# Kernel optimization log

Measured on AMD Instinct MI355X. Metric: run time of the kernel, lower is better.

Reference implementation:

```python
import jax, jax.numpy as jnp
import numpy as np

TARGET_SPARSITY = 0.9
LN_EPS = 1e-5


def ternary_quant(W):
    """BitNet-b1.58 style ternary quantization: W -> {-1,0,+1} * mean(|W|).
    Straight-through estimator so gradients pass to the latent weights."""
    scale = jnp.mean(jnp.abs(W))
    q = jnp.clip(jnp.round(W / (scale + 1e-8)), -1.0, 1.0) * scale
    return W + jax.lax.stop_gradient(q - W)


def layernorm(x, gamma, beta):
    mu = jnp.mean(x, axis=-1, keepdims=True)
    var = jnp.var(x, axis=-1, keepdims=True)
    return (x - mu) * jax.lax.rsqrt(var + LN_EPS) * gamma + beta


def setup_inputs() -> dict:
    key = jax.random.key(0)
    ks = jax.random.split(key, 3)
    B, S, D, N = 4, 2048, 2048, 8192
    x = jax.random.normal(ks[0], (B, S, D), dtype=jnp.float32)
    W_syn = jax.random.normal(ks[1], (N, D), dtype=jnp.float32) * (1.0 / np.sqrt(D))
    b_syn = jnp.zeros((N,), dtype=jnp.float32)
    W_out = jax.random.normal(ks[2], (D, N), dtype=jnp.float32) * (1.0 / np.sqrt(N))
    b_out = jnp.zeros((D,), dtype=jnp.float32)
    gamma = jnp.ones((D,), dtype=jnp.float32)
    beta = jnp.zeros((D,), dtype=jnp.float32)
    return {"x": x, "W_syn": W_syn, "b_syn": b_syn, "W_out": W_out,
            "b_out": b_out, "gamma": gamma, "beta": beta}


def reference(x, W_syn, b_syn, W_out, b_out, gamma, beta):
    B, S, D = x.shape
    N = W_syn.shape[0]
    x_flat = x.reshape(-1, D)  # [T, D], T = B*S

    # RNU: ternary-weight synapses + sparse firing (keep top (1-sparsity) per token)
    z = x_flat @ ternary_quant(W_syn).T + b_syn  # [T, N]
    k = max(1, int(N * (1.0 - TARGET_SPARSITY)))
    topv, _ = jax.lax.top_k(z, k)                 # [T, k]
    thresh = topv[:, -1:]                          # k-th largest per token
    hidden = jnp.where(z >= thresh, jax.nn.relu(z), 0.0)  # sparse firing rates

    # Ternary output projection
    out = hidden @ ternary_quant(W_out).T + b_out  # [T, D]
    out = out.reshape(B, S, D)

    # Residual + LayerNorm
    return layernorm(x + out, gamma, beta)
```

## Files before the change

### kernel.cpp

```cpp
#include <hip/hip_runtime.h>


typedef __attribute__((ext_vector_type(8))) short short8;
typedef __attribute__((ext_vector_type(4))) float f32x4;

__device__ __forceinline__ float bf2f(unsigned h) {
    return __uint_as_float(h << 16);
}
__device__ __forceinline__ unsigned f2bf(float f) {
    unsigned u = __float_as_uint(f);
    return (u + 0x7fffu + ((u >> 16) & 1u)) >> 16;
}

typedef __attribute__((address_space(1))) const void gq_void;
typedef __attribute__((address_space(3))) void ls_void;
__device__ __forceinline__ void gload16(const void* g, void* l) {
    __builtin_amdgcn_global_load_lds((gq_void*)g, (ls_void*)l, 16, 0, 0);
}

__global__ __launch_bounds__(64) void init_detect(float* sc, const unsigned* g_raw,
                                                  int* flag) {
    if (threadIdx.x < 16) sc[threadIdx.x] = 0.0f;
    if (threadIdx.x == 0) *flag = (g_raw[0] == 0x3F803F80u) ? 1 : 0;
}

__global__ __launch_bounds__(256) void split_x(const void* __restrict__ src,
                                               unsigned short* __restrict__ hi,
                                               unsigned short* __restrict__ lo, int n,
                                               const int* __restrict__ flagp) {
    const int flag = *flagp;
    int idx = blockIdx.x * 256 + threadIdx.x;
    int stride = gridDim.x * 256;
    if (flag) {
        const uint4* s = (const uint4*)src;
        uint4* dh = (uint4*)hi;
        uint4* dl = (uint4*)lo;
        uint4 zz; zz.x = zz.y = zz.z = zz.w = 0u;
        for (int i = idx; i < n / 8; i += stride) { dh[i] = s[i]; dl[i] = zz; }
    } else {
        const float4* s = (const float4*)src;
        uint2* dh = (uint2*)hi;
        uint2* dl = (uint2*)lo;
        for (int i = idx; i < n / 4; i += stride) {
            float4 v = s[i];
            unsigned h0 = f2bf(v.x), h1 = f2bf(v.y), h2 = f2bf(v.z), h3 = f2bf(v.w);
            unsigned l0 = f2bf(v.x - bf2f(h0));
            unsigned l1 = f2bf(v.y - bf2f(h1));
            unsigned l2 = f2bf(v.z - bf2f(h2));
            unsigned l3 = f2bf(v.w - bf2f(h3));
            uint2 oh; oh.x = h0 | (h1 << 16); oh.y = h2 | (h3 << 16);
            uint2 ol; ol.x = l0 | (l1 << 16); ol.y = l2 | (l3 << 16);
            dh[i] = oh;
            dl[i] = ol;
        }
    }
}

__global__ __launch_bounds__(256) void to_f32(const void* __restrict__ src,
                                              float* __restrict__ dst, int n,
                                              const int* __restrict__ flagp) {
    const int flag = *flagp;
    int i = blockIdx.x * 256 + threadIdx.x;
    if (i >= n) return;
    if (flag) dst[i] = bf2f((unsigned)((const unsigned short*)src)[i]);
    else dst[i] = ((const float*)src)[i];
}

__global__ __launch_bounds__(256) void abs_sum_any(const void* __restrict__ w, int n,
                                                   float* __restrict__ out,
                                                   const int* __restrict__ flagp) {
    const int flag = *flagp;
    int idx = blockIdx.x * 256 + threadIdx.x;
    int stride = gridDim.x * 256;
    float s = 0.0f;
    if (flag) {
        const uint4* wv = (const uint4*)w;
        for (int c = idx; c < n / 8; c += stride) {
            uint4 v = wv[c];
            unsigned a[4] = {v.x, v.y, v.z, v.w};
#pragma unroll
            for (int j = 0; j < 4; j++)
                s += fabsf(bf2f(a[j] & 0xffffu)) + fabsf(bf2f(a[j] >> 16));
        }
    } else {
        const float4* wv = (const float4*)w;
        for (int c = idx; c < n / 4; c += stride) {
            float4 v = wv[c];
            s += fabsf(v.x) + fabsf(v.y) + fabsf(v.z) + fabsf(v.w);
        }
    }
#pragma unroll
    for (int off = 32; off; off >>= 1) s += __shfl_down(s, off);
    __shared__ float red[4];
    int lane = threadIdx.x & 63, wv_id = threadIdx.x >> 6;
    if (lane == 0) red[wv_id] = s;
    __syncthreads();
    if (threadIdx.x == 0) atomicAdd(out, red[0] + red[1] + red[2] + red[3]);
}

__global__ __launch_bounds__(64) void finalize_scale(float* sc, float inv_count) {
    if (threadIdx.x == 0) {
        sc[2] = sc[0] * inv_count;
        sc[3] = sc[1] * inv_count;
    }
}

__global__ __launch_bounds__(256) void quantize_any(const void* __restrict__ w,
                                                    unsigned short* __restrict__ q,
                                                    const float* __restrict__ sc, int idx,
                                                    int n, const int* __restrict__ flagp) {
    const int flag = *flagp;
    const float d = sc[idx] + 1e-8f;
    int i = blockIdx.x * 256 + threadIdx.x;
    int stride = gridDim.x * 256;
    if (flag) {
        const uint4* wv = (const uint4*)w;
        uint4* qv = (uint4*)q;
        for (; i < n / 8; i += stride) {
            uint4 v = wv[i];
            unsigned a[4] = {v.x, v.y, v.z, v.w};
            unsigned r[4];
#pragma unroll
            for (int j = 0; j < 4; j++) {
                float lo = bf2f(a[j] & 0xffffu);
                float hi = bf2f(a[j] >> 16);
                float rl = fminf(1.0f, fmaxf(-1.0f, rintf(lo / d)));
                float rh = fminf(1.0f, fmaxf(-1.0f, rintf(hi / d)));
                r[j] = f2bf(rl) | (f2bf(rh) << 16);
            }
            uint4 o;
            o.x = r[0]; o.y = r[1]; o.z = r[2]; o.w = r[3];
            qv[i] = o;
        }
    } else {
        const float4* wv = (const float4*)w;
        uint2* qv = (uint2*)q;
        for (; i < n / 4; i += stride) {
            float4 v = wv[i];
            float r0 = fminf(1.0f, fmaxf(-1.0f, rintf(v.x / d)));
            float r1 = fminf(1.0f, fmaxf(-1.0f, rintf(v.y / d)));
            float r2 = fminf(1.0f, fmaxf(-1.0f, rintf(v.z / d)));
            float r3 = fminf(1.0f, fmaxf(-1.0f, rintf(v.w / d)));
            uint2 o;
            o.x = f2bf(r0) | (f2bf(r1) << 16);
            o.y = f2bf(r2) | (f2bf(r3) << 16);
            qv[i] = o;
        }
    }
}

template <int BM, int BN, bool TWO, int KSPLIT>
__global__ __launch_bounds__(256) void gemm_bt_t(const unsigned short* __restrict__ A0,
                                                 const unsigned short* __restrict__ A1,
                                                 const unsigned short* __restrict__ B,
                                                 float* __restrict__ C,
                                                 float* __restrict__ C2,
                                                 const float* __restrict__ biasf,
                                                 const float* __restrict__ scp, int scidx,
                                                 int N, int K) {
    constexpr int WM = BM / 2;
    constexpr int WN = BN / 2;
    constexpr int AM = WM / 16;
    constexpr int AN = WN / 16;
    __shared__ uint4 sA[BM * 8];
    __shared__ uint4 sL[TWO ? BM * 8 : 4];
    __shared__ uint4 sB[BN * 8];
    const int tid = threadIdx.x;
    const int lane = tid & 63;
    const int wave = tid >> 6;
    const int wm = (wave >> 1) * WM;
    const int wn = (wave & 1) * WN;
    const int m0 = blockIdx.y * BM;
    const int n0 = blockIdx.x * BN;
    const int l15 = lane & 15;
    const int quad = lane >> 4;

    const int kz = (KSPLIT > 1) ? (int)blockIdx.z : 0;
    const int kper = K / KSPLIT;
    const int kbeg = kz * kper;
    const int kend = kbeg + kper;
    float* __restrict__ Cw = (kz == 0) ? C : C2;

    f32x4 acc[AM][AN];
#pragma unroll
    for (int i = 0; i < AM; i++)
#pragma unroll
        for (int j = 0; j < AN; j++) acc[i][j] = (f32x4){0.f, 0.f, 0.f, 0.f};

    const unsigned short* Abase = A0 + (size_t)m0 * K;
    const unsigned short* Lbase = TWO ? (A1 + (size_t)m0 * K) : nullptr;
    const unsigned short* Bbase = B + (size_t)n0 * K;

    for (int k0 = kbeg; k0 < kend; k0 += 64) {
#pragma unroll
        for (int i = 0; i < BM * 8 / 256; i++) {
            int s = tid + i * 256;
            int r = s >> 3, c = s & 7;
            size_t go = (size_t)r * K + k0 + c * 8;
            gload16(Abase + go, sA + i * 256 + wave * 64);
            if (TWO) gload16(Lbase + go, sL + i * 256 + wave * 64);
        }
#pragma unroll
        for (int i = 0; i < BN * 8 / 256; i++) {
            int s = tid + i * 256;
            int r = s >> 3, c = s & 7;
            size_t go = (size_t)r * K + k0 + c * 8;
            gload16(Bbase + go, sB + i * 256 + wave * 64);
        }
        __syncthreads();
#pragma unroll
        for (int kk = 0; kk < 64; kk += 32) {
            const int jj = (kk >> 3) + quad;
            short8 ah[AM], bfr[AN];
#pragma unroll
            for (int t = 0; t < AM; t++)
                ah[t] = *(const short8*)&sA[(wm + t * 16 + l15) * 8 + jj];
#pragma unroll
            for (int t = 0; t < AN; t++)
                bfr[t] = *(const short8*)&sB[(wn + t * 16 + l15) * 8 + jj];
#pragma unroll
            for (int im = 0; im < AM; im++)
#pragma unroll
                for (int in = 0; in < AN; in++)
                    acc[im][in] = __builtin_amdgcn_mfma_f32_16x16x32_bf16(
                        ah[im], bfr[in], acc[im][in], 0, 0, 0);
            if (TWO) {
                short8 al[AM];
#pragma unroll
                for (int t = 0; t < AM; t++)
                    al[t] = *(const short8*)&sL[(wm + t * 16 + l15) * 8 + jj];
#pragma unroll
                for (int im = 0; im < AM; im++)
#pragma unroll
                    for (int in = 0; in < AN; in++)
                        acc[im][in] = __builtin_amdgcn_mfma_f32_16x16x32_bf16(
                            al[im], bfr[in], acc[im][in], 0, 0, 0);
            }
        }
        __syncthreads();
    }

    float scale = scp[scidx];
#pragma unroll
    for (int in = 0; in < AN; in++) {
        int col = n0 + wn + in * 16 + l15;
        float bv = (kz == 0) ? biasf[col] : 0.0f;
#pragma unroll
        for (int im = 0; im < AM; im++) {
            int rbase = m0 + wm + im * 16 + quad * 4;
#pragma unroll
            for (int r = 0; r < 4; r++) {
                Cw[(size_t)(rbase + r) * N + col] = scale * acc[im][in][r] + bv;
            }
        }
    }
}

__global__ __launch_bounds__(256) void topk_hidden(const float* __restrict__ z,
                                                   unsigned short* __restrict__ hidden,
                                                   int N, int k) {
    __shared__ unsigned keys[8192];
    __shared__ unsigned hist[2048];
    __shared__ unsigned csum[256];
    __shared__ unsigned sh_want, sh_kk;
    const int tid = threadIdx.x;
    const size_t row = blockIdx.x;
    const float* zr = z + row * (size_t)N;

    for (int i = tid; i < N; i += 256) {
        unsigned u = __float_as_uint(zr[i]);
        keys[i] = (u & 0x80000000u) ? ~u : (u | 0x80000000u);
    }
    if (tid == 0) { sh_want = 0u; sh_kk = (unsigned)k; }
    __syncthreads();

    for (int p = 0; p < 3; p++) {
        const int shift = (p == 0) ? 21 : (p == 1) ? 10 : 0;
        const int bits = (p == 2) ? 10 : 11;
        const int nb = 1 << bits;
        const unsigned want = sh_want;
        const unsigned kk = sh_kk;
        const int hs = shift + bits;
        for (int b = tid; b < nb; b += 256) hist[b] = 0u;
        __syncthreads();
        for (int i = tid; i < N; i += 256) {
            unsigned u = keys[i];
            bool match = (hs >= 32) ? true : ((u >> hs) == (want >> hs));
            if (match) atomicAdd(&hist[(u >> shift) & (nb - 1)], 1u);
        }
        __syncthreads();
        const int cs = nb >> 8;
        unsigned cv = 0;
        for (int j = 0; j < cs; j++) cv += hist[tid * cs + j];
        csum[tid] = cv;
        __syncthreads();
        for (int off = 1; off < 256; off <<= 1) {
            unsigned add = (tid + off < 256) ? csum[tid + off] : 0u;
            __syncthreads();
            csum[tid] += add;
            __syncthreads();
        }
        unsigned excl = (tid < 255) ? csum[tid + 1] : 0u;
        if (excl < kk && kk <= csum[tid]) {
            unsigned running = excl;
            for (int b = tid * cs + cs - 1; b >= tid * cs; b--) {
                unsigned h = hist[b];
                if (running + h >= kk) {
                    sh_want = want | ((unsigned)b << shift);
                    sh_kk = kk - running;
                    break;
                }
                running += h;
            }
        }
        __syncthreads();
    }

    const unsigned kth = sh_want;
    unsigned short* hr = hidden + row * (size_t)N;
    for (int i = tid; i < N; i += 256) {
        unsigned u = keys[i];
        float f = (u & 0x80000000u) ? __uint_as_float(u & 0x7fffffffu)
                                    : __uint_as_float(~u);
        float h = (u >= kth) ? fmaxf(f, 0.0f) : 0.0f;
        hr[i] = (unsigned short)f2bf(h);
    }
}

__global__ __launch_bounds__(256) void ln_kernel(const unsigned short* __restrict__ xh,
                                                 const unsigned short* __restrict__ xl,
                                                 const float* __restrict__ o,
                                                 const float* __restrict__ o2,
                                                 const float* __restrict__ gamma,
                                                 const float* __restrict__ beta,
                                                 float* __restrict__ y, int D) {
    const int tid = threadIdx.x;
    const size_t row = blockIdx.x;
    const unsigned short* xhr = xh + row * (size_t)D;
    const unsigned short* xlr = xl + row * (size_t)D;
    const float* orow = o + row * (size_t)D;
    const float* orow2 = o2 + row * (size_t)D;
    float v[8];
    float s = 0.0f, s2 = 0.0f;
#pragma unroll
    for (int j = 0; j < 8; j++) {
        int i = tid + j * 256;
        float val = bf2f((unsigned)xhr[i]) + bf2f((unsigned)xlr[i]) + orow[i] + orow2[i];
        v[j] = val;
        s += val;
        s2 += val * val;
    }
#pragma unroll
    for (int off = 32; off; off >>= 1) {
        s += __shfl_down(s, off);
        s2 += __shfl_down(s2, off);
    }
    __shared__ float red[8];
    int lane = tid & 63, wv = tid >> 6;
    if (lane == 0) { red[wv] = s; red[4 + wv] = s2; }
    __syncthreads();
    float S = red[0] + red[1] + red[2] + red[3];
    float S2 = red[4] + red[5] + red[6] + red[7];
    float mu = S / (float)D;
    float var = S2 / (float)D - mu * mu;
    float inv = rsqrtf(var + 1e-5f);
#pragma unroll
    for (int j = 0; j < 8; j++) {
        int i = tid + j * 256;
        y[row * (size_t)D + i] = (v[j] - mu) * inv * gamma[i] + beta[i];
    }
}

extern "C" void kernel_launch(void* const* d_in, const int* in_sizes, int n_in,
                              void* d_out, int out_size, void* d_ws, size_t ws_size,
                              hipStream_t stream) {
    const void* x_raw = d_in[0];
    const void* Wsyn_raw = d_in[1];
    const void* bsyn_raw = d_in[2];
    const void* Wout_raw = d_in[3];
    const void* bout_raw = d_in[4];
    const void* gamma_raw = d_in[5];
    const void* beta_raw = d_in[6];
    float* out = (float*)d_out;

    const int M = 8192, D = 2048, N = 8192, K1 = 2048;
    const int kTop = 819;
    const int NW = M * D;

    char* wsb = (char*)d_ws;
    float* sc = (float*)wsb;
    int* flag = (int*)(wsb + 128);
    float* gamma_f = (float*)(wsb + 4096);
    float* beta_f = (float*)(wsb + 12288);
    float* bout_f = (float*)(wsb + 20480);
    float* bsyn_f = (float*)(wsb + 28672);
    unsigned short* x_hi = (unsigned short*)(wsb + 65536);
    unsigned short* x_lo = (unsigned short*)(wsb + 65536 + 1ull * 33554432ull);
    unsigned short* qsyn = (unsigned short*)(wsb + 65536 + 2ull * 33554432ull);
    unsigned short* qout = (unsigned short*)(wsb + 65536 + 3ull * 33554432ull);
    const size_t FIXED = 65536 + 4ull * 33554432ull;

    const size_t per_row = (size_t)N * 4 + (size_t)N * 2;
    size_t avail = (ws_size > FIXED) ? ws_size - FIXED : 0;
    long mc = (long)(avail / per_row);
    mc &= ~127L;
    if (mc > M) mc = M;
    if (mc < 128) mc = 128;
    const int Mc = (int)mc;
    char* chunk_base = wsb + FIXED;

    init_detect<<<1, 64, 0, stream>>>(sc, (const unsigned*)gamma_raw, flag);

    split_x<<<2048, 256, 0, stream>>>(x_raw, x_hi, x_lo, M * D, flag);
    to_f32<<<(N + 255) / 256, 256, 0, stream>>>(bsyn_raw, bsyn_f, N, flag);
    to_f32<<<(D + 255) / 256, 256, 0, stream>>>(bout_raw, bout_f, D, flag);
    to_f32<<<(D + 255) / 256, 256, 0, stream>>>(gamma_raw, gamma_f, D, flag);
    to_f32<<<(D + 255) / 256, 256, 0, stream>>>(beta_raw, beta_f, D, flag);

    abs_sum_any<<<2048, 256, 0, stream>>>(Wsyn_raw, NW, sc + 0, flag);
    abs_sum_any<<<2048, 256, 0, stream>>>(Wout_raw, NW, sc + 1, flag);
    finalize_scale<<<1, 64, 0, stream>>>(sc, 1.0f / 16777216.0f);
    quantize_any<<<2048, 256, 0, stream>>>(Wsyn_raw, qsyn, sc, 2, NW, flag);
    quantize_any<<<2048, 256, 0, stream>>>(Wout_raw, qout, sc, 3, NW, flag);

    for (int m0 = 0; m0 < M; m0 += Mc) {
        const int rows = (M - m0 < Mc) ? (M - m0) : Mc;
        float* z = (float*)chunk_base;
        unsigned short* hidden = (unsigned short*)(chunk_base + (size_t)Mc * N * 4);
        float* outf = (float*)chunk_base;
        float* outf2 = (float*)(chunk_base + (size_t)rows * D * 4);

        dim3 g1(N / 128, rows / 128);
        gemm_bt_t<128, 128, true, 1><<<g1, 256, 0, stream>>>(
            x_hi + (size_t)m0 * K1, x_lo + (size_t)m0 * K1, qsyn, z, nullptr, bsyn_f,
            sc, 2, N, K1);

        topk_hidden<<<rows, 256, 0, stream>>>(z, hidden, N, kTop);

        dim3 g2(D / 64, rows / 128, 2);
        gemm_bt_t<128, 64, false, 2><<<g2, 256, 0, stream>>>(
            hidden, nullptr, qout, outf, outf2, bout_f, sc, 3, D, N);

        ln_kernel<<<rows, 256, 0, stream>>>(x_hi + (size_t)m0 * D, x_lo + (size_t)m0 * D,
                                            outf, outf2, gamma_f, beta_f,
                                            out + (size_t)m0 * D, D);
    }
}
```

Baseline: 1.804 ms.

## Streamline top-k radix select and retile output GEMM with four-way K split

The top-k kernel now builds the first histogram while loading keys with vectorised loads. It replaces the block-wide scan with wave shuffles, and finishes the third radix pass with a small candidate rank sort when the bucket holds few elements. The output projection GEMM moves from 128x64 tiles with a K-split of 2 to 128x128 tiles with a K-split of 4. Partial results are written to strided buffers that the layernorm kernel sums. This aims to cut top-k latency and improve GEMM tile reuse, at the cost of more partial-sum memory traffic in layernorm.

```diff
diff --git a/kernel.cpp b/kernel.cpp
--- a/kernel.cpp
+++ b/kernel.cpp
@@ -153,8 +153,7 @@
 __global__ __launch_bounds__(256) void gemm_bt_t(const unsigned short* __restrict__ A0,
                                                  const unsigned short* __restrict__ A1,
                                                  const unsigned short* __restrict__ B,
-                                                 float* __restrict__ C,
-                                                 float* __restrict__ C2,
+                                                 float* __restrict__ C, size_t cstride,
                                                  const float* __restrict__ biasf,
                                                  const float* __restrict__ scp, int scidx,
                                                  int N, int K) {
@@ -179,7 +178,7 @@
     const int kper = K / KSPLIT;
     const int kbeg = kz * kper;
     const int kend = kbeg + kper;
-    float* __restrict__ Cw = (kz == 0) ? C : C2;
+    float* __restrict__ Cw = C + (size_t)kz * cstride;
 
     f32x4 acc[AM][AN];
 #pragma unroll
@@ -261,76 +260,144 @@
                                                    int N, int k) {
     __shared__ unsigned keys[8192];
     __shared__ unsigned hist[2048];
-    __shared__ unsigned csum[256];
-    __shared__ unsigned sh_want, sh_kk;
+    __shared__ unsigned wsum[4];
+    __shared__ unsigned cand[256];
+    __shared__ unsigned sh_want, sh_kk, sh_cnt, sh_nc, sh_kth;
     const int tid = threadIdx.x;
+    const int lane = tid & 63;
+    const int wv = tid >> 6;
     const size_t row = blockIdx.x;
     const float* zr = z + row * (size_t)N;
 
-    for (int i = tid; i < N; i += 256) {
-        unsigned u = __float_as_uint(zr[i]);
-        keys[i] = (u & 0x80000000u) ? ~u : (u | 0x80000000u);
-    }
-    if (tid == 0) { sh_want = 0u; sh_kk = (unsigned)k; }
-    __syncthreads();
-
-    for (int p = 0; p < 3; p++) {
-        const int shift = (p == 0) ? 21 : (p == 1) ? 10 : 0;
-        const int bits = (p == 2) ? 10 : 11;
-        const int nb = 1 << bits;
-        const unsigned want = sh_want;
-        const unsigned kk = sh_kk;
-        const int hs = shift + bits;
-        for (int b = tid; b < nb; b += 256) hist[b] = 0u;
-        __syncthreads();
-        for (int i = tid; i < N; i += 256) {
-            unsigned u = keys[i];
-            bool match = (hs >= 32) ? true : ((u >> hs) == (want >> hs));
-            if (match) atomicAdd(&hist[(u >> shift) & (nb - 1)], 1u);
-        }
-        __syncthreads();
-        const int cs = nb >> 8;
+    auto select_bucket = [&](int nbins, int shift) {
+        const int cs = nbins >> 8;
+        const int base = tid * cs;
         unsigned cv = 0;
-        for (int j = 0; j < cs; j++) cv += hist[tid * cs + j];
-        csum[tid] = cv;
-        __syncthreads();
-        for (int off = 1; off < 256; off <<= 1) {
-            unsigned add = (tid + off < 256) ? csum[tid + off] : 0u;
-            __syncthreads();
-            csum[tid] += add;
-            __syncthreads();
-        }
-        unsigned excl = (tid < 255) ? csum[tid + 1] : 0u;
-        if (excl < kk && kk <= csum[tid]) {
+        for (int j = 0; j < cs; j++) cv += hist[base + j];
+        unsigned v = cv;
+#pragma unroll
+        for (int off = 1; off < 64; off <<= 1) {
+            unsigned o = __shfl_down(v, off);
+            if (lane + off < 64) v += o;
+        }
+        unsigned kk = sh_kk;
+        if (lane == 0) wsum[wv] = v;
+        __syncthreads();
+        unsigned higher = 0;
+        for (int w = wv + 1; w < 4; w++) higher += wsum[w];
+        unsigned incl = v + higher;
+        unsigned excl = incl - cv;
+        if (excl < kk && kk <= incl) {
             unsigned running = excl;
-            for (int b = tid * cs + cs - 1; b >= tid * cs; b--) {
+            for (int b = base + cs - 1; b >= base; b--) {
                 unsigned h = hist[b];
                 if (running + h >= kk) {
-                    sh_want = want | ((unsigned)b << shift);
+                    sh_want = sh_want | ((unsigned)b << shift);
                     sh_kk = kk - running;
+                    sh_cnt = h;
                     break;
                 }
                 running += h;
             }
         }
         __syncthreads();
-    }
-
-    const unsigned kth = sh_want;
+    };
+
+    for (int b = tid; b < 2048; b += 256) hist[b] = 0u;
+    if (tid == 0) { sh_want = 0u; sh_kk = (unsigned)k; }
+    __syncthreads();
+    const float4* zv = (const float4*)zr;
+    for (int i = tid; i < N / 4; i += 256) {
+        float4 f = zv[i];
+        unsigned u0 = __float_as_uint(f.x); u0 = (u0 & 0x80000000u) ? ~u0 : (u0 | 0x80000000u);
+        unsigned u1 = __float_as_uint(f.y); u1 = (u1 & 0x80000000u) ? ~u1 : (u1 | 0x80000000u);
+        unsigned u2 = __float_as_uint(f.z); u2 = (u2 & 0x80000000u) ? ~u2 : (u2 | 0x80000000u);
+        unsigned u3 = __float_as_uint(f.w); u3 = (u3 & 0x80000000u) ? ~u3 : (u3 | 0x80000000u);
+        keys[i * 4 + 0] = u0; keys[i * 4 + 1] = u1;
+        keys[i * 4 + 2] = u2; keys[i * 4 + 3] = u3;
+        atomicAdd(&hist[u0 >> 21], 1u);
+        atomicAdd(&hist[u1 >> 21], 1u);
+        atomicAdd(&hist[u2 >> 21], 1u);
+        atomicAdd(&hist[u3 >> 21], 1u);
+    }
+    __syncthreads();
+    select_bucket(2048, 21);
+
+    for (int b = tid; b < 2048; b += 256) hist[b] = 0u;
+    __syncthreads();
+    {
+        const unsigned want0 = sh_want;
+        for (int i = tid; i < N; i += 256) {
+            unsigned u = keys[i];
+            if ((u >> 21) == (want0 >> 21)) atomicAdd(&hist[(u >> 10) & 2047u], 1u);
+        }
+    }
+    __syncthreads();
+    select_bucket(2048, 10);
+
+    const unsigned want = sh_want;
+    const unsigned cnt = sh_cnt;
+    if (tid == 0) sh_nc = 0u;
+    __syncthreads();
+    if (cnt <= 256u) {
+        for (int i = tid; i < N; i += 256) {
+            unsigned u = keys[i];
+            if ((u >> 10) == (want >> 10)) {
+                unsigned p = atomicAdd(&sh_nc, 1u);
+                if (p < 256u) cand[p] = u;
+            }
+        }
+        __syncthreads();
+        const unsigned kk = sh_kk;
+        const int nc = (int)sh_nc;
+        if (tid < nc) {
+            unsigned vvv = cand[tid];
+            unsigned g = 0, ge = 0;
+            for (int j = 0; j < nc; j++) {
+                g += (cand[j] > vvv) ? 1u : 0u;
+                ge += (cand[j] >= vvv) ? 1u : 0u;
+            }
+            if (g < kk && kk <= ge) sh_kth = vvv;
+        }
+        __syncthreads();
+    } else {
+        for (int b = tid; b < 1024; b += 256) hist[b] = 0u;
+        __syncthreads();
+        for (int i = tid; i < N; i += 256) {
+            unsigned u = keys[i];
+            if ((u >> 10) == (want >> 10)) atomicAdd(&hist[u & 1023u], 1u);
+        }
+        __syncthreads();
+        select_bucket(1024, 0);
+        if (tid == 0) sh_kth = sh_want;
+        __syncthreads();
+    }
+    const unsigned kth = sh_kth;
+
     unsigned short* hr = hidden + row * (size_t)N;
-    for (int i = tid; i < N; i += 256) {
-        unsigned u = keys[i];
-        float f = (u & 0x80000000u) ? __uint_as_float(u & 0x7fffffffu)
-                                    : __uint_as_float(~u);
-        float h = (u >= kth) ? fmaxf(f, 0.0f) : 0.0f;
-        hr[i] = (unsigned short)f2bf(h);
+    uint2* hr2 = (uint2*)hr;
+    for (int i = tid; i < N / 4; i += 256) {
+        unsigned u0 = keys[i * 4 + 0], u1 = keys[i * 4 + 1];
+        unsigned u2 = keys[i * 4 + 2], u3 = keys[i * 4 + 3];
+        float f0 = (u0 & 0x80000000u) ? __uint_as_float(u0 & 0x7fffffffu) : __uint_as_float(~u0);
+        float f1 = (u1 & 0x80000000u) ? __uint_as_float(u1 & 0x7fffffffu) : __uint_as_float(~u1);
+        float f2 = (u2 & 0x80000000u) ? __uint_as_float(u2 & 0x7fffffffu) : __uint_as_float(~u2);
+        float f3 = (u3 & 0x80000000u) ? __uint_as_float(u3 & 0x7fffffffu) : __uint_as_float(~u3);
+        float h0 = (u0 >= kth) ? fmaxf(f0, 0.0f) : 0.0f;
+        float h1 = (u1 >= kth) ? fmaxf(f1, 0.0f) : 0.0f;
+        float h2 = (u2 >= kth) ? fmaxf(f2, 0.0f) : 0.0f;
+        float h3 = (u3 >= kth) ? fmaxf(f3, 0.0f) : 0.0f;
+        uint2 o;
+        o.x = f2bf(h0) | (f2bf(h1) << 16);
+        o.y = f2bf(h2) | (f2bf(h3) << 16);
+        hr2[i] = o;
     }
 }
 
 __global__ __launch_bounds__(256) void ln_kernel(const unsigned short* __restrict__ xh,
                                                  const unsigned short* __restrict__ xl,
                                                  const float* __restrict__ o,
-                                                 const float* __restrict__ o2,
+                                                 size_t cstride,
                                                  const float* __restrict__ gamma,
                                                  const float* __restrict__ beta,
                                                  float* __restrict__ y, int D) {
@@ -339,13 +406,13 @@
     const unsigned short* xhr = xh + row * (size_t)D;
     const unsigned short* xlr = xl + row * (size_t)D;
     const float* orow = o + row * (size_t)D;
-    const float* orow2 = o2 + row * (size_t)D;
     float v[8];
     float s = 0.0f, s2 = 0.0f;
 #pragma unroll
     for (int j = 0; j < 8; j++) {
         int i = tid + j * 256;
-        float val = bf2f((unsigned)xhr[i]) + bf2f((unsigned)xlr[i]) + orow[i] + orow2[i];
+        float val = bf2f((unsigned)xhr[i]) + bf2f((unsigned)xlr[i]);
+        val += orow[i] + orow[i + cstride] + orow[i + 2 * cstride] + orow[i + 3 * cstride];
         v[j] = val;
         s += val;
         s2 += val * val;
@@ -428,21 +495,21 @@
         float* z = (float*)chunk_base;
         unsigned short* hidden = (unsigned short*)(chunk_base + (size_t)Mc * N * 4);
         float* outf = (float*)chunk_base;
-        float* outf2 = (float*)(chunk_base + (size_t)rows * D * 4);
+        const size_t cstride = (size_t)rows * D;
 
         dim3 g1(N / 128, rows / 128);
         gemm_bt_t<128, 128, true, 1><<<g1, 256, 0, stream>>>(
-            x_hi + (size_t)m0 * K1, x_lo + (size_t)m0 * K1, qsyn, z, nullptr, bsyn_f,
+            x_hi + (size_t)m0 * K1, x_lo + (size_t)m0 * K1, qsyn, z, 0, bsyn_f,
             sc, 2, N, K1);
 
         topk_hidden<<<rows, 256, 0, stream>>>(z, hidden, N, kTop);
 
-        dim3 g2(D / 64, rows / 128, 2);
-        gemm_bt_t<128, 64, false, 2><<<g2, 256, 0, stream>>>(
-            hidden, nullptr, qout, outf, outf2, bout_f, sc, 3, D, N);
+        dim3 g2(D / 128, rows / 128, 4);
+        gemm_bt_t<128, 128, false, 4><<<g2, 256, 0, stream>>>(
+            hidden, nullptr, qout, outf, cstride, bout_f, sc, 3, D, N);
 
         ln_kernel<<<rows, 256, 0, stream>>>(x_hi + (size_t)m0 * D, x_lo + (size_t)m0 * D,
-                                            outf, outf2, gamma_f, beta_f,
+                                            outf, cstride, gamma_f, beta_f,
                                             out + (size_t)m0 * D, D);
     }
 }
```

After: 1.751 ms. 1.03x faster.
